# Kernel optimization log

Hardware: AMD Instinct MI355X
Metric: run time of the kernel (lower is better)

## Reference

```python
import jax, jax.numpy as jnp
import numpy as np

FEAT_DIM = 128
CUTOFF = 5.0


def setup_inputs() -> dict:
    key = jax.random.key(0)
    ks = jax.random.split(key, 12)
    B, NA, NC, F = 2, 1500, 64, FEAT_DIM
    inp = {
        "assign": jax.random.randint(ks[0], (B, NA), 0, NC),
        "h": jax.random.normal(ks[1], (B, NA, F), dtype=jnp.float32),
        "H": jax.random.normal(ks[2], (B, NC, F), dtype=jnp.float32),
        "cg_xyz": jax.random.normal(ks[3], (B, NC, 3), dtype=jnp.float32) * 3.0,
        "xyz": jax.random.normal(ks[4], (B, NA, 3), dtype=jnp.float32) * 3.0,
        "cg_adj": jax.random.uniform(ks[5], (B, NC, NC), dtype=jnp.float32),
        # dist_filter: Dense(F -> 3F)
        "Wf": jax.random.normal(ks[6], (F, 3 * F), dtype=jnp.float32) / np.sqrt(F),
        "bf": jnp.zeros((3 * F,), dtype=jnp.float32),
        # inv_dense: Dense(F->F, swish) -> Dense(F->3F)
        "W1": jax.random.normal(ks[7], (F, F), dtype=jnp.float32) / np.sqrt(F),
        "b1": jnp.zeros((F,), dtype=jnp.float32),
        "W2": jax.random.normal(ks[8], (F, 3 * F), dtype=jnp.float32) / np.sqrt(F),
        "b2": jnp.zeros((3 * F,), dtype=jnp.float32),
    }
    return inp


def reference(assign, h, H, cg_xyz, xyz, cg_adj, Wf, bf, W1, b1, W2, b2):
    F = h.shape[-1]
    # pairwise displacement: [B, n_cg, n_atoms, 3]
    r_iI = xyz[:, None, :, :] - cg_xyz[:, :, None, :]
    d_iI = jnp.sqrt(jnp.sum(r_iI * r_iI, axis=-1))          # [B, nc, na]
    unit = r_iI / d_iI[..., None]                            # [B, nc, na, 3]
    offset = jnp.linspace(0.0, CUTOFF, F)                    # [F]
    # invariant branch on atom features: swish MLP -> 3F
    phi = jax.nn.silu(h @ W1 + b1) @ W2 + b2                 # [B, na, 3F]
    # Gaussian RBF expansion of distances
    expanded_dist = jnp.exp(-jnp.square(d_iI[..., None] - offset))  # [B, nc, na, F]
    w_s = expanded_dist @ Wf + bf                            # [B, nc, na, 3F]
    filter_w = (w_s * phi[:, None, :, :]).reshape(*w_s.shape[:-1], F, 3)
    split_1 = filter_w[..., 1]                               # [B, nc, na, F]
    split_2 = filter_w[..., 2]                               # [B, nc, na, F]
    # v_i is all-zeros in the original, so the split_0 * v_i term vanishes
    unit_add = split_2[..., None] * unit[..., None, :]       # [B, nc, na, F, 3]
    dV = unit_add.sum(axis=2)                                # [B, nc, F, 3]
    dH = split_1.sum(axis=2)                                 # [B, nc, F]
    return (H + dH, dV)  # V_I is zeros, so V_I + dV == dV
```

## Files before the change

### kernel.cpp

```cpp
#include <hip/hip_runtime.h>
#include <cmath>

#define FDIM 128
#define NPTS 64
#define TDLT 0.16f
#define INVTDLT 6.25f
#define CLAMPF 62.0f

typedef __attribute__((ext_vector_type(8))) __bf16 bf16x8;
typedef __attribute__((ext_vector_type(4))) float f32x4;

__device__ inline unsigned short f2bf(float x) {
  unsigned int u = __float_as_uint(x);
  return (unsigned short)((u + 0x7FFFu + ((u >> 16) & 1u)) >> 16);
}
__device__ inline float bfw_lo(unsigned int w) { return __uint_as_float(w << 16); }
__device__ inline float bfw_hi(unsigned int w) { return __uint_as_float(w & 0xFFFF0000u); }
__device__ inline float rdlane(float v, int j) {
  return __int_as_float(__builtin_amdgcn_readlane(__float_as_int(v), j));
}

__global__ __launch_bounds__(256) void prep_kernel(
    const float* __restrict__ W1, const float* __restrict__ W2,
    const float* __restrict__ Wf, const float* __restrict__ bf,
    unsigned short* __restrict__ W1f, unsigned short* __restrict__ W2f,
    unsigned int* __restrict__ Tq) {
  const int bid = blockIdx.x;
  const int tid = threadIdx.x;
  if (bid < 128) {
    if (tid >= 64) return;
    const int ft = bid & 15, kt = (bid >> 4) & 3, z = bid >> 6;
    const int lane = tid;
    const float* W;
    unsigned short* out;
    int col, stride;
    if (z == 0) {
      if (ft >= 8) return;
      W = W1; out = W1f; col = ft * 16 + (lane & 15); stride = 128;
    } else {
      W = W2; out = W2f;
      col = 3 * ((ft & 7) * 16 + (lane & 15)) + 1 + (ft >> 3);
      stride = 384;
    }
    unsigned short g[8];
#pragma unroll
    for (int j = 0; j < 8; ++j) {
      const int k = kt * 32 + ((lane >> 4) << 3) + j;
      g[j] = f2bf(W[(size_t)k * stride + col]);
    }
    uint4 u;
    u.x = g[0] | ((unsigned int)g[1] << 16);
    u.y = g[2] | ((unsigned int)g[3] << 16);
    u.z = g[4] | ((unsigned int)g[5] << 16);
    u.w = g[6] | ((unsigned int)g[7] << 16);
    *(uint4*)&out[((size_t)(ft * 4 + kt) * 64 + lane) * 8] = u;
  } else {
    __shared__ float g[128];
    __shared__ float part[2][128][2];
    const int pt = bid - 128;
    const int f = tid & 127;
    const int kh = tid >> 7;
    if (tid < 128) {
      const float dpt = pt * TDLT;
      const float o = tid * (5.0f / 127.0f);
      const float dd = dpt - o;
      g[tid] = expf(-dd * dd);
    }
    __syncthreads();
    float s0 = 0.f, s1 = 0.f;
#pragma unroll 8
    for (int kk = 0; kk < 64; ++kk) {
      const int k = kh * 64 + kk;
      s0 = fmaf(g[k], Wf[(size_t)k * 384 + 3 * f + 1], s0);
      s1 = fmaf(g[k], Wf[(size_t)k * 384 + 3 * f + 2], s1);
    }
    part[kh][f][0] = s0;
    part[kh][f][1] = s1;
    __syncthreads();
    if (tid < 128) {
      const float v0 = part[0][tid][0] + part[1][tid][0] + bf[3 * tid + 1];
      const float v1 = part[0][tid][1] + part[1][tid][1] + bf[3 * tid + 2];
      const unsigned int word = f2bf(v0) | ((unsigned int)f2bf(v1) << 16);
      Tq[((size_t)pt * 64 + (tid & 63)) * 2 + (tid >> 6)] = word;
    }
  }
}

__global__ __launch_bounds__(256) void phi_mfma_kernel(
    const float* __restrict__ h, const unsigned short* __restrict__ W1f,
    const float* __restrict__ b1, const unsigned short* __restrict__ W2f,
    const float* __restrict__ b2, unsigned int* __restrict__ phiQ, int BNA) {
  __shared__ __bf16 hA[4 * 64 * 8];
  __shared__ unsigned short tS[16 * 128];
  const int tid = threadIdx.x;
  const int lane = tid & 63;
  const int w = tid >> 6;
  const int hw = lane >> 4, lcol = lane & 15;
  const int r0 = blockIdx.x * 16;

  {
    const int gl = tid & 63;
    const int kt = tid >> 6;
    const int row = gl & 15;
    const int k0 = kt * 32 + ((gl >> 4) << 3);
    const int gr = r0 + row;
    bf16x8 v;
    if (gr < BNA) {
      const float4 f0 = *(const float4*)&h[(size_t)gr * FDIM + k0];
      const float4 f1 = *(const float4*)&h[(size_t)gr * FDIM + k0 + 4];
      v[0] = (__bf16)f0.x; v[1] = (__bf16)f0.y; v[2] = (__bf16)f0.z; v[3] = (__bf16)f0.w;
      v[4] = (__bf16)f1.x; v[5] = (__bf16)f1.y; v[6] = (__bf16)f1.z; v[7] = (__bf16)f1.w;
    } else {
#pragma unroll
      for (int j = 0; j < 8; ++j) v[j] = (__bf16)0.0f;
    }
    *reinterpret_cast<bf16x8*>(&hA[tid * 8]) = v;
  }

  bf16x8 B1[2][4];
#pragma unroll
  for (int ftl = 0; ftl < 2; ++ftl)
#pragma unroll
    for (int kt = 0; kt < 4; ++kt)
      B1[ftl][kt] = *reinterpret_cast<const bf16x8*>(
          &W1f[(((size_t)(w * 2 + ftl) * 4 + kt) * 64 + lane) * 8]);
  float b1v[2];
#pragma unroll
  for (int ftl = 0; ftl < 2; ++ftl) b1v[ftl] = b1[w * 32 + ftl * 16 + lcol];
  __syncthreads();

  {
    bf16x8 ga[4];
#pragma unroll
    for (int kt = 0; kt < 4; ++kt)
      ga[kt] = *reinterpret_cast<const bf16x8*>(&hA[(kt * 64 + lane) * 8]);
    f32x4 acc[2];
    acc[0] = (f32x4){0.f, 0.f, 0.f, 0.f};
    acc[1] = (f32x4){0.f, 0.f, 0.f, 0.f};
#pragma unroll
    for (int ftl = 0; ftl < 2; ++ftl)
#pragma unroll
      for (int kt = 0; kt < 4; ++kt)
        acc[ftl] = __builtin_amdgcn_mfma_f32_16x16x32_bf16(ga[kt], B1[ftl][kt], acc[ftl], 0, 0, 0);
#pragma unroll
    for (int ftl = 0; ftl < 2; ++ftl)
#pragma unroll
      for (int reg = 0; reg < 4; ++reg) {
        const int row = hw * 4 + reg;
        const int fcol = w * 32 + ftl * 16 + lcol;
        const float x = acc[ftl][reg] + b1v[ftl];
        const float t = x / (1.0f + __expf(-x));
        const int byte = (row * 256 + fcol * 2) ^ ((row & 7) << 4);
        *(unsigned short*)((char*)tS + byte) = f2bf(t);
      }
  }

  bf16x8 B2[2][2][4];
  float b2v[2][2];
#pragma unroll
  for (int ftl = 0; ftl < 2; ++ftl) {
    const int fcol = w * 32 + ftl * 16 + lcol;
#pragma unroll
    for (int s_ = 0; s_ < 2; ++s_) {
      const int ft = s_ * 8 + w * 2 + ftl;
#pragma unroll
      for (int kt = 0; kt < 4; ++kt)
        B2[ftl][s_][kt] = *reinterpret_cast<const bf16x8*>(
            &W2f[(((size_t)ft * 4 + kt) * 64 + lane) * 8]);
      b2v[ftl][s_] = b2[3 * fcol + 1 + s_];
    }
  }
  __syncthreads();

  {
    bf16x8 ta[4];
#pragma unroll
    for (int kt = 0; kt < 4; ++kt) {
      const int row = lcol;
      const int k0 = kt * 32 + hw * 8;
      const int byte = (row * 256 + k0 * 2) ^ ((row & 7) << 4);
      ta[kt] = *reinterpret_cast<const bf16x8*>((const char*)tS + byte);
    }
    f32x4 acc[2][2];
#pragma unroll
    for (int ftl = 0; ftl < 2; ++ftl)
#pragma unroll
      for (int s_ = 0; s_ < 2; ++s_) acc[ftl][s_] = (f32x4){0.f, 0.f, 0.f, 0.f};
#pragma unroll
    for (int ftl = 0; ftl < 2; ++ftl)
#pragma unroll
      for (int s_ = 0; s_ < 2; ++s_)
#pragma unroll
        for (int kt = 0; kt < 4; ++kt)
          acc[ftl][s_] = __builtin_amdgcn_mfma_f32_16x16x32_bf16(ta[kt], B2[ftl][s_][kt],
                                                                 acc[ftl][s_], 0, 0, 0);
#pragma unroll
    for (int ftl = 0; ftl < 2; ++ftl)
#pragma unroll
      for (int reg = 0; reg < 4; ++reg) {
        const int row = hw * 4 + reg;
        const int gr = r0 + row;
        if (gr < BNA) {
          const float v0 = acc[ftl][0][reg] + b2v[ftl][0];
          const float v1 = acc[ftl][1][reg] + b2v[ftl][1];
          const unsigned int word = f2bf(v0) | ((unsigned int)f2bf(v1) << 16);
          phiQ[(size_t)gr * FDIM + w * 32 + ftl * 16 + lcol] = word;
        }
      }
  }
}

template <int ASPLIT>
__global__ __launch_bounds__(512, 6) void enc_main_kernel(
    const float* __restrict__ xyz, const float* __restrict__ cg_xyz,
    const unsigned int* __restrict__ Tg, const unsigned int* __restrict__ phiQ,
    float* __restrict__ pH, float* __restrict__ pV,
    int NA, int NC, int BNC, int BNA) {
  __shared__ uint2 Tl[NPTS * 64];

  const int az = blockIdx.x;
  const int c = blockIdx.y;
  const int b = blockIdx.z;
  const int bc = b * NC + c;
  const int tid = threadIdx.x;
  const int l = tid & 63;
  const int wv = tid >> 6;
  const size_t arow = (size_t)b * NA;

  {
    const uint4* src4 = (const uint4*)Tg;
    uint4* dst4 = (uint4*)Tl;
#pragma unroll
    for (int i = 0; i < 4; ++i) dst4[tid + i * 512] = src4[tid + i * 512];
  }

  const float cgx = cg_xyz[bc * 3 + 0];
  const float cgy = cg_xyz[bc * 3 + 1];
  const float cgz = cg_xyz[bc * 3 + 2];

  const int APA = (NA + ASPLIT - 1) / ASPLIT;
  const int a0 = az * APA;
  const int a_end = min(NA, a0 + APA);
  const int cnt = (a_end > a0) ? (a_end - a0) : 0;
  const int wcnt = (cnt + 7) >> 3;
  const int aw0 = a0 + wv * wcnt;
  const int aw1 = min(a_end, aw0 + wcnt);

  __syncthreads();

  float accH0 = 0.f, accH1 = 0.f;
  float accV0[3] = {0.f, 0.f, 0.f};
  float accV1[3] = {0.f, 0.f, 0.f};

  for (int base = aw0; base < aw1; base += 64) {
    int n = aw1 - base;
    if (n > 64) n = 64;

    float fidx = 0.f, ux = 0.f, uy = 0.f, uz = 0.f;
    if (l < n) {
      const int a = base + l;
      const float dx = xyz[(arow + a) * 3 + 0] - cgx;
      const float dy = xyz[(arow + a) * 3 + 1] - cgy;
      const float dz = xyz[(arow + a) * 3 + 2] - cgz;
      const float d = sqrtf(dx * dx + dy * dy + dz * dz);
      const float inv = 1.0f / d;
      ux = dx * inv; uy = dy * inv; uz = dz * inv;
      fidx = fminf(d * INVTDLT, CLAMPF);
    }

    const unsigned int* pq = phiQ + ((size_t)(arow + base)) * FDIM + l;

    for (int jb = 0; jb < n; jb += 4) {
      uint2 t0[4], t1[4];
      float fr[4], sux[4], suy[4], suz[4];
      unsigned int pa[4], pb[4];
#pragma unroll
      for (int q = 0; q < 4; ++q) {
        const int jj = jb + q;
        const int jl = jj & 63;
        const float sf = rdlane(fidx, jl);
        const int idx = (int)sf;
        fr[q] = sf - (float)idx;
        t0[q] = Tl[idx * 64 + l];
        t1[q] = Tl[idx * 64 + 64 + l];
        sux[q] = rdlane(ux, jl);
        suy[q] = rdlane(uy, jl);
        suz[q] = rdlane(uz, jl);
        if (jj < n) {
          pa[q] = pq[(size_t)jj * FDIM];
          pb[q] = pq[(size_t)jj * FDIM + 64];
        } else {
          pa[q] = 0u; pb[q] = 0u;
        }
      }
#pragma unroll
      for (int q = 0; q < 4; ++q) {
        const float A1 = bfw_lo(t0[q].x), A2 = bfw_hi(t0[q].x);
        const float B1 = bfw_lo(t1[q].x), B2 = bfw_hi(t1[q].x);
        const float C1 = bfw_lo(t0[q].y), C2 = bfw_hi(t0[q].y);
        const float D1 = bfw_lo(t1[q].y), D2 = bfw_hi(t1[q].y);
        const float S1a = fmaf(fr[q], B1 - A1, A1);
        const float S2a = fmaf(fr[q], B2 - A2, A2);
        const float S1b = fmaf(fr[q], D1 - C1, C1);
        const float S2b = fmaf(fr[q], D2 - C2, C2);

        const float p1a = bfw_lo(pa[q]), p2a = bfw_hi(pa[q]);
        const float p1b = bfw_lo(pb[q]), p2b = bfw_hi(pb[q]);

        accH0 = fmaf(S1a, p1a, accH0);
        accH1 = fmaf(S1b, p1b, accH1);
        const float t2a = S2a * p2a;
        const float t2b = S2b * p2b;
        accV0[0] = fmaf(t2a, sux[q], accV0[0]);
        accV0[1] = fmaf(t2a, suy[q], accV0[1]);
        accV0[2] = fmaf(t2a, suz[q], accV0[2]);
        accV1[0] = fmaf(t2b, sux[q], accV1[0]);
        accV1[1] = fmaf(t2b, suy[q], accV1[1]);
        accV1[2] = fmaf(t2b, suz[q], accV1[2]);
      }
    }
  }

  __syncthreads();
  float* red = (float*)Tl;
  red[0 * 512 + wv * 64 + l] = accH0;
  red[1 * 512 + wv * 64 + l] = accH1;
  red[2 * 512 + wv * 64 + l] = accV0[0];
  red[3 * 512 + wv * 64 + l] = accV0[1];
  red[4 * 512 + wv * 64 + l] = accV0[2];
  red[5 * 512 + wv * 64 + l] = accV1[0];
  red[6 * 512 + wv * 64 + l] = accV1[1];
  red[7 * 512 + wv * 64 + l] = accV1[2];
  __syncthreads();
  {
    const int comp = tid >> 6;
    const int sl = tid & 63;
    float v = 0.f;
#pragma unroll
    for (int w8 = 0; w8 < 8; ++w8) v += red[comp * 512 + w8 * 64 + sl];
    if (comp == 0) {
      pH[((size_t)az * BNC + bc) * FDIM + sl] = v;
    } else if (comp == 1) {
      pH[((size_t)az * BNC + bc) * FDIM + sl + 64] = v;
    } else if (comp < 5) {
      pV[(((size_t)az * BNC + bc) * FDIM + sl) * 3 + (comp - 2)] = v;
    } else {
      pV[(((size_t)az * BNC + bc) * FDIM + sl + 64) * 3 + (comp - 5)] = v;
    }
  }
}

template <int P>
__global__ __launch_bounds__(FDIM) void reduce_kernel(
    const float* __restrict__ H, const float* __restrict__ pH, const float* __restrict__ pV,
    float* __restrict__ out, int BNC) {
  const int bc = blockIdx.x;
  const int f = threadIdx.x;
  float s = H[(size_t)bc * FDIM + f];
#pragma unroll
  for (int p = 0; p < P; ++p) s += pH[((size_t)p * BNC + bc) * FDIM + f];
  out[(size_t)bc * FDIM + f] = s;
  float* outV = out + (size_t)BNC * FDIM;
#pragma unroll
  for (int x = 0; x < 3; ++x) {
    float v = 0.f;
#pragma unroll
    for (int p = 0; p < P; ++p) v += pV[(((size_t)p * BNC + bc) * FDIM + f) * 3 + x];
    outV[((size_t)bc * FDIM + f) * 3 + x] = v;
  }
}

extern "C" void kernel_launch(void* const* d_in, const int* in_sizes, int n_in,
                              void* d_out, int out_size, void* d_ws, size_t ws_size,
                              hipStream_t stream) {
  const float* h      = (const float*)d_in[1];
  const float* Hc     = (const float*)d_in[2];
  const float* cg_xyz = (const float*)d_in[3];
  const float* xyz    = (const float*)d_in[4];
  const float* Wf     = (const float*)d_in[6];
  const float* bf     = (const float*)d_in[7];
  const float* W1     = (const float*)d_in[8];
  const float* b1     = (const float*)d_in[9];
  const float* W2     = (const float*)d_in[10];
  const float* b2     = (const float*)d_in[11];

  const int BNC = in_sizes[2] / FDIM;
  const int NC  = in_sizes[5] / BNC;
  const int B   = BNC / NC;
  const int NA  = in_sizes[0] / B;
  const int BNA = B * NA;
  constexpr int ASPLIT = 4;

  char* wsb = (char*)d_ws;
  unsigned short* W1f = (unsigned short*)wsb;
  unsigned short* W2f = (unsigned short*)(wsb + 32768);
  unsigned int*  Tq   = (unsigned int*)(wsb + 32768 + 65536);
  unsigned int*  phiQ = (unsigned int*)(wsb + 2 * 65536);
  char* pp = wsb + 2 * 65536 + (size_t)BNA * FDIM * 4;
  float* pH = (float*)pp;                  pp += (size_t)ASPLIT * BNC * FDIM * 4;
  float* pV = (float*)pp;

  prep_kernel<<<128 + NPTS, 256, 0, stream>>>(W1, W2, Wf, bf, W1f, W2f, Tq);
  phi_mfma_kernel<<<(BNA + 15) / 16, 256, 0, stream>>>(h, W1f, b1, W2f, b2, phiQ, BNA);
  enc_main_kernel<ASPLIT><<<dim3(ASPLIT, NC, B), 512, 0, stream>>>(
      xyz, cg_xyz, Tq, phiQ, pH, pV, NA, NC, BNC, BNA);
  reduce_kernel<ASPLIT><<<BNC, FDIM, 0, stream>>>(Hc, pH, pV, (float*)d_out, BNC);
}
```

Measured before the change: 33.23 us.

## Merge weight prep and phi MLP into one launch, interleave phi for uint2 loads

The separate weight-packing kernel is removed. Each phi block now converts its W1/W2 fragments to bf16 directly from global memory, and the RBF table build runs as extra blocks in the same launch, which cuts one kernel launch and its dependency. phiQ is stored interleaved so the main kernel fetches both feature halves with a single 8-byte load, and the table index and fraction are computed once per atom before broadcasting. ASPLIT is raised from 4 to 6 for more parallelism, at the cost of more partial sums to reduce and redundant strided weight reads in every phi block.

```diff
diff --git a/kernel.cpp b/kernel.cpp
--- a/kernel.cpp
+++ b/kernel.cpp
@@ -20,44 +20,19 @@
   return __int_as_float(__builtin_amdgcn_readlane(__float_as_int(v), j));
 }
 
-__global__ __launch_bounds__(256) void prep_kernel(
+__global__ __launch_bounds__(256) void combo_kernel(
     const float* __restrict__ W1, const float* __restrict__ W2,
     const float* __restrict__ Wf, const float* __restrict__ bf,
-    unsigned short* __restrict__ W1f, unsigned short* __restrict__ W2f,
-    unsigned int* __restrict__ Tq) {
+    const float* __restrict__ h, const float* __restrict__ b1,
+    const float* __restrict__ b2,
+    unsigned int* __restrict__ Tq, unsigned int* __restrict__ phiQ2, int BNA) {
   const int bid = blockIdx.x;
   const int tid = threadIdx.x;
-  if (bid < 128) {
-    if (tid >= 64) return;
-    const int ft = bid & 15, kt = (bid >> 4) & 3, z = bid >> 6;
-    const int lane = tid;
-    const float* W;
-    unsigned short* out;
-    int col, stride;
-    if (z == 0) {
-      if (ft >= 8) return;
-      W = W1; out = W1f; col = ft * 16 + (lane & 15); stride = 128;
-    } else {
-      W = W2; out = W2f;
-      col = 3 * ((ft & 7) * 16 + (lane & 15)) + 1 + (ft >> 3);
-      stride = 384;
-    }
-    unsigned short g[8];
-#pragma unroll
-    for (int j = 0; j < 8; ++j) {
-      const int k = kt * 32 + ((lane >> 4) << 3) + j;
-      g[j] = f2bf(W[(size_t)k * stride + col]);
-    }
-    uint4 u;
-    u.x = g[0] | ((unsigned int)g[1] << 16);
-    u.y = g[2] | ((unsigned int)g[3] << 16);
-    u.z = g[4] | ((unsigned int)g[5] << 16);
-    u.w = g[6] | ((unsigned int)g[7] << 16);
-    *(uint4*)&out[((size_t)(ft * 4 + kt) * 64 + lane) * 8] = u;
-  } else {
+
+  if (bid < NPTS) {
     __shared__ float g[128];
     __shared__ float part[2][128][2];
-    const int pt = bid - 128;
+    const int pt = bid;
     const int f = tid & 127;
     const int kh = tid >> 7;
     if (tid < 128) {
@@ -83,20 +58,15 @@
       const unsigned int word = f2bf(v0) | ((unsigned int)f2bf(v1) << 16);
       Tq[((size_t)pt * 64 + (tid & 63)) * 2 + (tid >> 6)] = word;
     }
-  }
-}
-
-__global__ __launch_bounds__(256) void phi_mfma_kernel(
-    const float* __restrict__ h, const unsigned short* __restrict__ W1f,
-    const float* __restrict__ b1, const unsigned short* __restrict__ W2f,
-    const float* __restrict__ b2, unsigned int* __restrict__ phiQ, int BNA) {
+    return;
+  }
+
   __shared__ __bf16 hA[4 * 64 * 8];
   __shared__ unsigned short tS[16 * 128];
-  const int tid = threadIdx.x;
   const int lane = tid & 63;
   const int w = tid >> 6;
   const int hw = lane >> 4, lcol = lane & 15;
-  const int r0 = blockIdx.x * 16;
+  const int r0 = (bid - NPTS) * 16;
 
   {
     const int gl = tid & 63;
@@ -119,11 +89,14 @@
 
   bf16x8 B1[2][4];
 #pragma unroll
-  for (int ftl = 0; ftl < 2; ++ftl)
+  for (int ftl = 0; ftl < 2; ++ftl) {
+    const int col = w * 32 + ftl * 16 + lcol;
 #pragma unroll
     for (int kt = 0; kt < 4; ++kt)
-      B1[ftl][kt] = *reinterpret_cast<const bf16x8*>(
-          &W1f[(((size_t)(w * 2 + ftl) * 4 + kt) * 64 + lane) * 8]);
+#pragma unroll
+      for (int j = 0; j < 8; ++j)
+        B1[ftl][kt][j] = (__bf16)W1[(size_t)(kt * 32 + hw * 8 + j) * FDIM + col];
+  }
   float b1v[2];
 #pragma unroll
   for (int ftl = 0; ftl < 2; ++ftl) b1v[ftl] = b1[w * 32 + ftl * 16 + lcol];
@@ -162,12 +135,13 @@
     const int fcol = w * 32 + ftl * 16 + lcol;
 #pragma unroll
     for (int s_ = 0; s_ < 2; ++s_) {
-      const int ft = s_ * 8 + w * 2 + ftl;
+      const int col = 3 * fcol + 1 + s_;
 #pragma unroll
       for (int kt = 0; kt < 4; ++kt)
-        B2[ftl][s_][kt] = *reinterpret_cast<const bf16x8*>(
-            &W2f[(((size_t)ft * 4 + kt) * 64 + lane) * 8]);
-      b2v[ftl][s_] = b2[3 * fcol + 1 + s_];
+#pragma unroll
+        for (int j = 0; j < 8; ++j)
+          B2[ftl][s_][kt][j] = (__bf16)W2[(size_t)(kt * 32 + hw * 8 + j) * 384 + col];
+      b2v[ftl][s_] = b2[col];
     }
   }
   __syncthreads();
@@ -201,10 +175,11 @@
         const int row = hw * 4 + reg;
         const int gr = r0 + row;
         if (gr < BNA) {
+          const int fcol = w * 32 + ftl * 16 + lcol;
           const float v0 = acc[ftl][0][reg] + b2v[ftl][0];
           const float v1 = acc[ftl][1][reg] + b2v[ftl][1];
           const unsigned int word = f2bf(v0) | ((unsigned int)f2bf(v1) << 16);
-          phiQ[(size_t)gr * FDIM + w * 32 + ftl * 16 + lcol] = word;
+          phiQ2[(size_t)gr * FDIM + (fcol & 63) * 2 + (fcol >> 6)] = word;
         }
       }
   }
@@ -213,7 +188,7 @@
 template <int ASPLIT>
 __global__ __launch_bounds__(512, 6) void enc_main_kernel(
     const float* __restrict__ xyz, const float* __restrict__ cg_xyz,
-    const unsigned int* __restrict__ Tg, const unsigned int* __restrict__ phiQ,
+    const unsigned int* __restrict__ Tg, const uint2* __restrict__ phiQ2,
     float* __restrict__ pH, float* __restrict__ pV,
     int NA, int NC, int BNC, int BNA) {
   __shared__ uint2 Tl[NPTS * 64];
@@ -256,7 +231,8 @@
     int n = aw1 - base;
     if (n > 64) n = 64;
 
-    float fidx = 0.f, ux = 0.f, uy = 0.f, uz = 0.f;
+    int idxl = 0;
+    float frl = 0.f, ux = 0.f, uy = 0.f, uz = 0.f;
     if (l < n) {
       const int a = base + l;
       const float dx = xyz[(arow + a) * 3 + 0] - cgx;
@@ -265,32 +241,31 @@
       const float d = sqrtf(dx * dx + dy * dy + dz * dz);
       const float inv = 1.0f / d;
       ux = dx * inv; uy = dy * inv; uz = dz * inv;
-      fidx = fminf(d * INVTDLT, CLAMPF);
-    }
-
-    const unsigned int* pq = phiQ + ((size_t)(arow + base)) * FDIM + l;
+      const float sf = fminf(d * INVTDLT, CLAMPF);
+      idxl = (int)sf;
+      frl = sf - (float)idxl;
+    }
+
+    const uint2* pq2 = phiQ2 + ((size_t)(arow + base)) * 64 + l;
 
     for (int jb = 0; jb < n; jb += 4) {
-      uint2 t0[4], t1[4];
+      uint2 t0[4], t1[4], pv[4];
       float fr[4], sux[4], suy[4], suz[4];
-      unsigned int pa[4], pb[4];
 #pragma unroll
       for (int q = 0; q < 4; ++q) {
         const int jj = jb + q;
         const int jl = jj & 63;
-        const float sf = rdlane(fidx, jl);
-        const int idx = (int)sf;
-        fr[q] = sf - (float)idx;
+        const int idx = __builtin_amdgcn_readlane(idxl, jl);
+        fr[q] = rdlane(frl, jl);
         t0[q] = Tl[idx * 64 + l];
         t1[q] = Tl[idx * 64 + 64 + l];
         sux[q] = rdlane(ux, jl);
         suy[q] = rdlane(uy, jl);
         suz[q] = rdlane(uz, jl);
         if (jj < n) {
-          pa[q] = pq[(size_t)jj * FDIM];
-          pb[q] = pq[(size_t)jj * FDIM + 64];
+          pv[q] = pq2[(size_t)jj * 64];
         } else {
-          pa[q] = 0u; pb[q] = 0u;
+          pv[q].x = 0u; pv[q].y = 0u;
         }
       }
 #pragma unroll
@@ -304,8 +279,8 @@
         const float S1b = fmaf(fr[q], D1 - C1, C1);
         const float S2b = fmaf(fr[q], D2 - C2, C2);
 
-        const float p1a = bfw_lo(pa[q]), p2a = bfw_hi(pa[q]);
-        const float p1b = bfw_lo(pb[q]), p2b = bfw_hi(pb[q]);
+        const float p1a = bfw_lo(pv[q].x), p2a = bfw_hi(pv[q].x);
+        const float p1b = bfw_lo(pv[q].y), p2b = bfw_hi(pv[q].y);
 
         accH0 = fmaf(S1a, p1a, accH0);
         accH1 = fmaf(S1b, p1b, accH1);
@@ -389,20 +364,19 @@
   const int B   = BNC / NC;
   const int NA  = in_sizes[0] / B;
   const int BNA = B * NA;
-  constexpr int ASPLIT = 4;
+  constexpr int ASPLIT = 6;
 
   char* wsb = (char*)d_ws;
-  unsigned short* W1f = (unsigned short*)wsb;
-  unsigned short* W2f = (unsigned short*)(wsb + 32768);
-  unsigned int*  Tq   = (unsigned int*)(wsb + 32768 + 65536);
-  unsigned int*  phiQ = (unsigned int*)(wsb + 2 * 65536);
-  char* pp = wsb + 2 * 65536 + (size_t)BNA * FDIM * 4;
+  unsigned int* Tq    = (unsigned int*)wsb;
+  unsigned int* phiQ2 = (unsigned int*)(wsb + 32768);
+  char* pp = wsb + 32768 + (size_t)BNA * FDIM * 4;
   float* pH = (float*)pp;                  pp += (size_t)ASPLIT * BNC * FDIM * 4;
   float* pV = (float*)pp;
 
-  prep_kernel<<<128 + NPTS, 256, 0, stream>>>(W1, W2, Wf, bf, W1f, W2f, Tq);
-  phi_mfma_kernel<<<(BNA + 15) / 16, 256, 0, stream>>>(h, W1f, b1, W2f, b2, phiQ, BNA);
+  const int nphi = (BNA + 15) / 16;
+  combo_kernel<<<NPTS + nphi, 256, 0, stream>>>(W1, W2, Wf, bf, h, b1, b2,
+                                                Tq, phiQ2, BNA);
   enc_main_kernel<ASPLIT><<<dim3(ASPLIT, NC, B), 512, 0, stream>>>(
-      xyz, cg_xyz, Tq, phiQ, pH, pV, NA, NC, BNC, BNA);
+      xyz, cg_xyz, Tq, (const uint2*)phiQ2, pH, pV, NA, NC, BNC, BNA);
   reduce_kernel<ASPLIT><<<BNC, FDIM, 0, stream>>>(Hc, pH, pV, (float*)d_out, BNC);
 }
```

Result: faster. 30.37 us (-8.6%).
